# Kernel tuning notes

Hardware: AMD Instinct MI355X
Metric: run time of the kernel (lower is better)

The kernel has to match this reference:

```python
import jax, jax.numpy as jnp
import numpy as np

B, N, H, D, HS, RS = 4, 512, 16, 64, 1024, 64  # HS = H*D, HSIZE_INSIDE == HSIZE
SCALE = 1.0 / float(np.sqrt(D))


def setup_inputs() -> dict:
    key = jax.random.key(0)
    ks = jax.random.split(key, 11)
    s = 0.02
    return {
        "v": jax.random.normal(ks[0], (B, N, HS), jnp.float32),
        "k": jax.random.normal(ks[1], (B, N, HS), jnp.float32),
        "q": jax.random.normal(ks[2], (B, N, HS), jnp.float32),
        "mask": jax.random.randint(ks[3], (B, 1, N, N), 0, 2).astype(bool),
        "rel_embed": jax.random.uniform(ks[4], (B, N, N, RS), jnp.float32),
        # weights stored as [in, out] (torch Linear applies x @ W.T)
        "Wv": jax.random.normal(ks[5], (HS, HS), jnp.float32) * s,
        "Wk": jax.random.normal(ks[6], (HS, HS), jnp.float32) * s,
        "Wq": jax.random.normal(ks[7], (HS, HS), jnp.float32) * s,
        "Wr": jax.random.normal(ks[8], (RS, H), jnp.float32) * s,
        "br": jax.random.normal(ks[9], (H,), jnp.float32) * s,
        "Wm": jax.random.normal(ks[10], (HS, HS), jnp.float32) * s,
    }


def reference(v, k, q, mask, rel_embed, Wv, Wk, Wq, Wr, br, Wm):
    b, nq, _ = q.shape

    def proj(x, W):  # [b, n, HS] -> [b, H, n, D]
        return (x @ W).reshape(b, -1, H, D).transpose(0, 2, 1, 3)

    vh, kh, qh = proj(v, Wv), proj(k, Wk), proj(q, Wq)
    # learned relative-position bias: relu -> clamp -> log, [b, H, nq, nk]
    r = jax.nn.relu(rel_embed @ Wr + br)
    bias = jnp.log(jnp.clip(r, 1e-6, None)).transpose(0, 3, 1, 2)
    scores = jnp.einsum('bhqd,bhkd->bhqk', qh, kh) * SCALE + bias
    scores = jnp.where(mask, jnp.float32(-1e9), scores)
    att = jax.nn.softmax(scores, axis=-1)  # dropout_r = 0
    atted = jnp.einsum('bhqk,bhkd->bhqd', att, vh)
    atted = atted.transpose(0, 2, 1, 3).reshape(b, nq, H * D)
    return atted @ Wm
```

## Files before the change

### kernel.cpp

```cpp
#include <hip/hip_runtime.h>
#include <hip/hip_bf16.h>


typedef __bf16 bf16_t;
typedef __bf16 bf16x8 __attribute__((ext_vector_type(8)));
typedef float f32x4 __attribute__((ext_vector_type(4)));

__device__ __forceinline__ f32x4 mfma16(bf16x8 a, bf16x8 b, f32x4 c) {
  return __builtin_amdgcn_mfma_f32_16x16x32_bf16(a, b, c, 0, 0, 0);
}
__device__ __forceinline__ f32x4 zero4() {
  f32x4 z; z[0] = 0.f; z[1] = 0.f; z[2] = 0.f; z[3] = 0.f; return z;
}

#define GLOAD_LDS16(gptr, lptr)                                                   \
  __builtin_amdgcn_global_load_lds(                                               \
      (const __attribute__((address_space(1))) unsigned int*)(gptr),              \
      (__attribute__((address_space(3))) unsigned int*)(lptr), 16, 0, 0)

__global__ __launch_bounds__(256) void prep_kernel(
    const float* __restrict__ W0, const float* __restrict__ W1,
    const float* __restrict__ W2, const float* __restrict__ W3,
    bf16_t* __restrict__ OutBase,
    const float* __restrict__ q, const float* __restrict__ k, const float* __restrict__ v,
    bf16_t* __restrict__ Qc, bf16_t* __restrict__ Kc, bf16_t* __restrict__ Vc,
    const unsigned int* __restrict__ mw, int* __restrict__ flag) {
  const int tid = threadIdx.x;
  if (blockIdx.x >= 1024) {
    const size_t gid = (size_t)(blockIdx.x - 1024) * 256 + tid;
    const int which = (int)(gid >> 18);
    const size_t off = (gid & 262143) * 8;
    const float* src = which == 0 ? q : which == 1 ? k : v;
    bf16_t* dst = which == 0 ? Qc : which == 1 ? Kc : Vc;
    const float scl = which == 0 ? 0.125f : 1.0f;
    float4 f0 = *(const float4*)(src + off);
    float4 f1 = *(const float4*)(src + off + 4);
    bf16x8 o;
    o[0] = (bf16_t)(f0.x * scl); o[1] = (bf16_t)(f0.y * scl);
    o[2] = (bf16_t)(f0.z * scl); o[3] = (bf16_t)(f0.w * scl);
    o[4] = (bf16_t)(f1.x * scl); o[5] = (bf16_t)(f1.y * scl);
    o[6] = (bf16_t)(f1.z * scl); o[7] = (bf16_t)(f1.w * scl);
    *(bf16x8*)(dst + off) = o;
    return;
  }
  const int wz = blockIdx.x >> 8, wy = (blockIdx.x >> 4) & 15, wx = blockIdx.x & 15;
  const float* W = wz == 0 ? W0 : wz == 1 ? W1 : wz == 2 ? W2 : W3;
  bf16_t* Ot = OutBase + (size_t)wz * 1024 * 1024;
  __shared__ float tile[64][68];
  __shared__ int sflag;
  const bool probe = (blockIdx.x == 0);
  if (probe && tid == 0) sflag = 0;
  const int i0 = wy * 64, j0 = wx * 64;
  const int ri = tid >> 2, rc = (tid & 3) * 16;
  const float* src = W + (size_t)(i0 + ri) * 1024 + j0 + rc;
#pragma unroll
  for (int qq = 0; qq < 4; ++qq) {
    float4 f = *(const float4*)(src + qq * 4);
    *(float4*)(&tile[ri][rc + qq * 4]) = f;
  }
  if (probe) {
    int any = 0;
    for (int i = tid; i < 4096; i += 256) any |= (mw[i] > 1u) ? 1 : 0;
    if (any) atomicOr(&sflag, 1);
  }
  __syncthreads();
  const int wj = tid >> 2, wc = (tid & 3) * 16;
  bf16x8 o0, o1;
#pragma unroll
  for (int s = 0; s < 8; ++s) o0[s] = (bf16_t)tile[wc + s][wj];
#pragma unroll
  for (int s = 0; s < 8; ++s) o1[s] = (bf16_t)tile[wc + 8 + s][wj];
  bf16_t* dst = Ot + (size_t)(j0 + wj) * 1024 + i0 + wc;
  *(bf16x8*)dst = o0;
  *(bf16x8*)(dst + 8) = o1;
  if (probe && tid == 0) *flag = sflag;
}

__global__ __launch_bounds__(256) void fat_kernel(
    const float* __restrict__ rel, const float* __restrict__ Wr,
    const float* __restrict__ br, const void* __restrict__ mask,
    const int* __restrict__ mflag, bf16_t* __restrict__ biasM,
    const bf16_t* __restrict__ Aq, const bf16_t* __restrict__ Ak, const bf16_t* __restrict__ Av,
    const bf16_t* __restrict__ Bq, const bf16_t* __restrict__ Bk, const bf16_t* __restrict__ Bv,
    bf16_t* __restrict__ Oq, bf16_t* __restrict__ Ok, bf16_t* __restrict__ Ov) {
  __shared__ __align__(16) bf16_t Asm[128 * 64];
  __shared__ __align__(16) bf16_t Bsm[128 * 64];
  const int tid = threadIdx.x, wid = tid >> 6, lane = tid & 63;
  const int lg = lane >> 4, lc = lane & 15;

  if (blockIdx.x < 2048) {
    const int pair = blockIdx.x;
    const int b = pair >> 9, qrow = pair & 511;
    const int isU8 = *mflag;
    bf16x8 wf[2];
#pragma unroll
    for (int kk = 0; kk < 2; ++kk)
#pragma unroll
      for (int j = 0; j < 8; ++j)
        wf[kk][j] = (bf16_t)Wr[(kk * 32 + lg * 8 + j) * 16 + lc];
    float brv[4];
#pragma unroll
    for (int j = 0; j < 4; ++j) brv[j] = br[lg * 4 + j];
    const float* relrow = rel + (size_t)pair * 512 * 64;
    const size_t mbase = (size_t)b * 512 * 512 + (size_t)qrow * 512;
    bf16_t* outb = biasM + (size_t)b * 16 * 512 * 512 + (size_t)qrow * 512;
#pragma unroll 4
    for (int kt = wid * 8; kt < wid * 8 + 8; ++kt) {
      const int k0 = kt * 16;
      const float* rrow = relrow + (size_t)(k0 + lc) * 64;
      f32x4 acc;
      acc[0] = brv[0]; acc[1] = brv[1]; acc[2] = brv[2]; acc[3] = brv[3];
#pragma unroll
      for (int kk = 0; kk < 2; ++kk) {
        const float4* s = (const float4*)(rrow + kk * 32 + lg * 8);
        float4 f0 = s[0], f1 = s[1];
        bf16x8 bfr;
        bfr[0] = (bf16_t)f0.x; bfr[1] = (bf16_t)f0.y; bfr[2] = (bf16_t)f0.z; bfr[3] = (bf16_t)f0.w;
        bfr[4] = (bf16_t)f1.x; bfr[5] = (bf16_t)f1.y; bfr[6] = (bf16_t)f1.z; bfr[7] = (bf16_t)f1.w;
        acc = mfma16(wf[kk], bfr, acc);
      }
      bool mb;
      if (isU8) mb = ((const unsigned char*)mask)[mbase + k0 + lc] != 0;
      else      mb = ((const int*)mask)[mbase + k0 + lc] != 0;
#pragma unroll
      for (int j = 0; j < 4; ++j) {
        const float valf = mb ? -1e9f : __logf(fmaxf(acc[j], 1e-6f));
        outb[(size_t)(lg * 4 + j) * 512 * 512 + k0 + lc] = (bf16_t)valf;
      }
    }
    return;
  }

  const int idx = blockIdx.x - 2048;
  const int z = idx >> 7, rem = idx & 127;
  const int byy = rem >> 3, bxx = rem & 7;
  const bf16_t* A = (z == 0) ? Aq : (z == 1) ? Ak : Av;
  const bf16_t* Bt = (z == 0) ? Bq : (z == 1) ? Bk : Bv;
  bf16_t* Out = (z == 0) ? Oq : (z == 1) ? Ok : Ov;
  const int m0 = byy * 128, n0 = bxx * 128;
  const int wm = (wid >> 1) * 64, wn = (wid & 1) * 64;
  const int sr = lane >> 3;
  const int scch = lane & 7;
  const int srcch = scch ^ sr;
  const bf16_t* Ap[4];
  const bf16_t* Bp[4];
#pragma unroll
  for (int i = 0; i < 4; ++i) {
    const int r = wid * 32 + i * 8 + sr;
    Ap[i] = A + (size_t)(m0 + r) * 1024 + srcch * 8;
    Bp[i] = Bt + (size_t)(n0 + r) * 1024 + srcch * 8;
  }
  f32x4 acc[4][4];
#pragma unroll
  for (int i = 0; i < 4; ++i)
#pragma unroll
    for (int j = 0; j < 4; ++j) acc[i][j] = zero4();

  for (int k0 = 0; k0 < 1024; k0 += 64) {
#pragma unroll
    for (int i = 0; i < 4; ++i) {
      GLOAD_LDS16(Ap[i] + k0, Asm + (wid * 32 + i * 8) * 64);
      GLOAD_LDS16(Bp[i] + k0, Bsm + (wid * 32 + i * 8) * 64);
    }
    __syncthreads();
#pragma unroll
    for (int kk = 0; kk < 2; ++kk) {
      bf16x8 af[4], bfv[4];
#pragma unroll
      for (int i = 0; i < 4; ++i) {
        const int ar = wm + i * 16 + lc;
        af[i] = *(const bf16x8*)(Asm + ar * 64 + ((kk * 4 + lg) ^ (ar & 7)) * 8);
        const int brr = wn + i * 16 + lc;
        bfv[i] = *(const bf16x8*)(Bsm + brr * 64 + ((kk * 4 + lg) ^ (brr & 7)) * 8);
      }
#pragma unroll
      for (int mi = 0; mi < 4; ++mi)
#pragma unroll
        for (int ni = 0; ni < 4; ++ni) acc[mi][ni] = mfma16(af[mi], bfv[ni], acc[mi][ni]);
    }
    __syncthreads();
  }
#pragma unroll
  for (int mi = 0; mi < 4; ++mi)
#pragma unroll
    for (int ni = 0; ni < 4; ++ni)
#pragma unroll
      for (int j = 0; j < 4; ++j) {
        const int m = m0 + wm + mi * 16 + lg * 4 + j;
        const int col = n0 + wn + ni * 16 + lc;
        const int b = m >> 9, n = m & 511;
        const int h = col >> 6, d = col & 63;
        Out[(((size_t)(b * 16 + h)) * 512 + n) * 64 + d] = (bf16_t)acc[mi][ni][j];
      }
}

__global__ __launch_bounds__(256) void attn_kernel(
    const bf16_t* __restrict__ Qh, const bf16_t* __restrict__ Kh,
    const bf16_t* __restrict__ Vh, const bf16_t* __restrict__ biasM,
    bf16_t* __restrict__ atted) {
  __shared__ __align__(16) bf16_t Ksm[2][64 * 64];
  __shared__ __align__(16) bf16_t Vtsm[2][64 * 88];
  __shared__ __align__(16) bf16_t Psm[4 * 16 * 64];
  const int tid = threadIdx.x, wid = tid >> 6, lane = tid & 63;
  const int lg = lane >> 4, lc = lane & 15;
  const int bid = blockIdx.x;
  const int qt = bid & 7, h = (bid >> 3) & 15, b = bid >> 7;
  const size_t headoff = (size_t)(b * 16 + h) * 512 * 64;
  const bf16_t* Qb = Qh + headoff;
  const bf16_t* Kb = Kh + headoff;
  const bf16_t* Vb = Vh + headoff;
  const int q0 = qt * 64 + wid * 16;
  const bf16_t* biasb = biasM + ((size_t)(b * 16 + h) * 512 + q0) * 512;

  bf16x8 qf[2];
#pragma unroll
  for (int kk = 0; kk < 2; ++kk)
    qf[kk] = *(const bf16x8*)(Qb + (size_t)(q0 + lc) * 64 + kk * 32 + lg * 8);

  f32x4 Oacc[4];
#pragma unroll
  for (int ds = 0; ds < 4; ++ds) Oacc[ds] = zero4();
  float mrun[4], lrun[4];
#pragma unroll
  for (int j = 0; j < 4; ++j) { mrun[j] = -INFINITY; lrun[j] = 0.f; }

  const int krow = tid & 63, kc0 = (tid >> 6) * 2;
  const int vn = tid & 63, vd0 = (tid >> 6) * 16;
  bf16_t* Pw = Psm + wid * 16 * 64;

#define STAGE(T, BUF)                                                          \
  do {                                                                         \
    const int kb_ = (T) * 64;                                                  \
    _Pragma("unroll") for (int ci = 0; ci < 2; ++ci) {                         \
      const int c_ = kc0 + ci;                                                 \
      bf16x8 kv_ = *(const bf16x8*)(Kb + (size_t)(kb_ + krow) * 64 + c_ * 8);  \
      *(bf16x8*)(Ksm[BUF] + krow * 64 + (c_ ^ (krow & 7)) * 8) = kv_;          \
    }                                                                          \
    bf16x8 v0_ = *(const bf16x8*)(Vb + (size_t)(kb_ + vn) * 64 + vd0);         \
    bf16x8 v1_ = *(const bf16x8*)(Vb + (size_t)(kb_ + vn) * 64 + vd0 + 8);     \
    _Pragma("unroll") for (int i = 0; i < 8; ++i)                              \
        Vtsm[BUF][(vd0 + i) * 88 + vn] = v0_[i];                               \
    _Pragma("unroll") for (int i = 0; i < 8; ++i)                              \
        Vtsm[BUF][(vd0 + 8 + i) * 88 + vn] = v1_[i];                           \
  } while (0)

  STAGE(0, 0);
  __syncthreads();

  for (int t = 0; t < 8; ++t) {
    const int cur = t & 1;
    if (t < 7) STAGE(t + 1, cur ^ 1);

    f32x4 sacc[4];
#pragma unroll
    for (int quad = 0; quad < 4; ++quad)
#pragma unroll
      for (int j = 0; j < 4; ++j)
        sacc[quad][j] = (float)biasb[(size_t)(lg * 4 + j) * 512 + t * 64 + quad * 16 + lc];

    const bf16_t* Kc = Ksm[cur];
#pragma unroll
    for (int quad = 0; quad < 4; ++quad) {
      const int kr = quad * 16 + lc;
#pragma unroll
      for (int kk = 0; kk < 2; ++kk) {
        bf16x8 kf = *(const bf16x8*)(Kc + kr * 64 + ((kk * 4 + lg) ^ (kr & 7)) * 8);
        sacc[quad] = mfma16(qf[kk], kf, sacc[quad]);
      }
    }

    float p[4][4];
#pragma unroll
    for (int j = 0; j < 4; ++j) {
      float tmax = fmaxf(fmaxf(sacc[0][j], sacc[1][j]), fmaxf(sacc[2][j], sacc[3][j]));
#pragma unroll
      for (int mm = 1; mm < 16; mm <<= 1) tmax = fmaxf(tmax, __shfl_xor(tmax, mm));
      const float mnew = fmaxf(mrun[j], tmax);
      const float sf = __expf(mrun[j] - mnew);
      mrun[j] = mnew;
      lrun[j] *= sf;
#pragma unroll
      for (int ds = 0; ds < 4; ++ds) Oacc[ds][j] *= sf;
      float psum = 0.f;
#pragma unroll
      for (int quad = 0; quad < 4; ++quad) {
        const float pv = __expf(sacc[quad][j] - mnew);
        p[quad][j] = pv;
        psum += pv;
      }
      lrun[j] += psum;
    }

#pragma unroll
    for (int quad = 0; quad < 4; ++quad)
#pragma unroll
      for (int j = 0; j < 4; ++j) {
        const int row = lg * 4 + j, col = quad * 16 + lc;
        Pw[row * 64 + ((col >> 3) ^ (row & 7)) * 8 + (col & 7)] = (bf16_t)p[quad][j];
      }

    const bf16_t* Vc = Vtsm[cur];
#pragma unroll
    for (int kk = 0; kk < 2; ++kk) {
      bf16x8 pf = *(const bf16x8*)(Pw + lc * 64 + ((kk * 4 + lg) ^ (lc & 7)) * 8);
#pragma unroll
      for (int ds = 0; ds < 4; ++ds) {
        bf16x8 vf = *(const bf16x8*)(Vc + (ds * 16 + lc) * 88 + kk * 32 + lg * 8);
        Oacc[ds] = mfma16(pf, vf, Oacc[ds]);
      }
    }
    __syncthreads();
  }
#undef STAGE

#pragma unroll
  for (int j = 0; j < 4; ++j) {
    float l = lrun[j];
#pragma unroll
    for (int mm = 1; mm < 16; mm <<= 1) l += __shfl_xor(l, mm);
    lrun[j] = 1.0f / l;
  }
#pragma unroll
  for (int ds = 0; ds < 4; ++ds)
#pragma unroll
    for (int j = 0; j < 4; ++j) {
      const int n = q0 + lg * 4 + j;
      const int d = ds * 16 + lc;
      atted[((size_t)b * 512 + n) * 1024 + h * 64 + d] = (bf16_t)(Oacc[ds][j] * lrun[j]);
    }
}

__global__ __launch_bounds__(256) void out_gemm2(
    const bf16_t* __restrict__ A, const bf16_t* __restrict__ Bt, float* __restrict__ Out) {
  __shared__ __align__(16) bf16_t Asm[128 * 64];
  __shared__ __align__(16) bf16_t Bsm[128 * 64];
  const int tid = threadIdx.x, wid = tid >> 6, lane = tid & 63;
  const int lg = lane >> 4, lc = lane & 15;
  const int m0 = blockIdx.y * 128, n0 = blockIdx.x * 128;
  const int wm = (wid >> 1) * 64, wn = (wid & 1) * 64;
  const int sr = lane >> 3, scch = lane & 7;
  const int srcch = scch ^ sr;
  const bf16_t* Ap[4];
  const bf16_t* Bp[4];
#pragma unroll
  for (int i = 0; i < 4; ++i) {
    const int r = wid * 32 + i * 8 + sr;
    Ap[i] = A + (size_t)(m0 + r) * 1024 + srcch * 8;
    Bp[i] = Bt + (size_t)(n0 + r) * 1024 + srcch * 8;
  }
  f32x4 acc[4][4];
#pragma unroll
  for (int i = 0; i < 4; ++i)
#pragma unroll
    for (int j = 0; j < 4; ++j) acc[i][j] = zero4();

  for (int k0 = 0; k0 < 1024; k0 += 64) {
#pragma unroll
    for (int i = 0; i < 4; ++i) {
      GLOAD_LDS16(Ap[i] + k0, Asm + (wid * 32 + i * 8) * 64);
      GLOAD_LDS16(Bp[i] + k0, Bsm + (wid * 32 + i * 8) * 64);
    }
    __syncthreads();
#pragma unroll
    for (int kk = 0; kk < 2; ++kk) {
      bf16x8 af[4], bfv[4];
#pragma unroll
      for (int i = 0; i < 4; ++i) {
        const int ar = wm + i * 16 + lc;
        af[i] = *(const bf16x8*)(Asm + ar * 64 + ((kk * 4 + lg) ^ (ar & 7)) * 8);
        const int brr = wn + i * 16 + lc;
        bfv[i] = *(const bf16x8*)(Bsm + brr * 64 + ((kk * 4 + lg) ^ (brr & 7)) * 8);
      }
#pragma unroll
      for (int mi = 0; mi < 4; ++mi)
#pragma unroll
        for (int ni = 0; ni < 4; ++ni) acc[mi][ni] = mfma16(af[mi], bfv[ni], acc[mi][ni]);
    }
    __syncthreads();
  }
#pragma unroll
  for (int mi = 0; mi < 4; ++mi)
#pragma unroll
    for (int ni = 0; ni < 4; ++ni)
#pragma unroll
      for (int j = 0; j < 4; ++j) {
        const int m = m0 + wm + mi * 16 + lg * 4 + j;
        const int col = n0 + wn + ni * 16 + lc;
        Out[(size_t)m * 1024 + col] = acc[mi][ni][j];
      }
}

extern "C" void kernel_launch(void* const* d_in, const int* in_sizes, int n_in,
                              void* d_out, int out_size, void* d_ws, size_t ws_size,
                              hipStream_t stream) {
  const float* v = (const float*)d_in[0];
  const float* k = (const float*)d_in[1];
  const float* q = (const float*)d_in[2];
  const void* mask = d_in[3];
  const float* rel = (const float*)d_in[4];
  const float* Wv = (const float*)d_in[5];
  const float* Wk = (const float*)d_in[6];
  const float* Wq = (const float*)d_in[7];
  const float* Wr = (const float*)d_in[8];
  const float* br = (const float*)d_in[9];
  const float* Wm = (const float*)d_in[10];

  char* ws = (char*)d_ws;
  bf16_t* Wt = (bf16_t*)ws;
  bf16_t* Qh = (bf16_t*)(ws + ((size_t)8 << 20));
  bf16_t* Kh = (bf16_t*)(ws + ((size_t)12 << 20));
  bf16_t* Vh = (bf16_t*)(ws + ((size_t)16 << 20));
  bf16_t* biasM = (bf16_t*)(ws + ((size_t)20 << 20));
  bf16_t* atted = (bf16_t*)(ws + ((size_t)52 << 20));
  bf16_t* Qc = (bf16_t*)(ws + ((size_t)56 << 20));
  bf16_t* Kc = (bf16_t*)(ws + ((size_t)60 << 20));
  bf16_t* Vc = (bf16_t*)(ws + ((size_t)64 << 20));
  int* mflag = (int*)(ws + ((size_t)68 << 20));
  bf16_t* Wvt = Wt + 0 * 1048576;
  bf16_t* Wkt = Wt + 1 * 1048576;
  bf16_t* Wqt = Wt + 2 * 1048576;
  bf16_t* Wmt = Wt + 3 * 1048576;

  prep_kernel<<<dim3(4096), 256, 0, stream>>>(Wv, Wk, Wq, Wm, Wt, q, k, v, Qc, Kc, Vc,
                                              (const unsigned int*)mask, mflag);
  fat_kernel<<<dim3(2432), 256, 0, stream>>>(rel, Wr, br, mask, mflag, biasM,
                                             Qc, Kc, Vc, Wqt, Wkt, Wvt, Qh, Kh, Vh);
  attn_kernel<<<dim3(512), 256, 0, stream>>>(Qh, Kh, Vh, biasM, atted);
  out_gemm2<<<dim3(8, 16), 256, 0, stream>>>(atted, Wmt, (float*)d_out);
}
```

Before: 144.8 us.

## Split bias computation across prep and projection kernels, prefetch bias before staging

Moves the relative-position bias work so that 896 of the 2048 (batch, query-row) blocks run inside the prep kernel and the other 1152 run inside the projection GEMM kernel. The bias work, which mostly streams memory, then overlaps with both the weight transpose/convert and the GEMM. The mask dtype probe now runs per block on its own mask row instead of as a single global flag, removing the dependency on the prep kernel. In attention, bias loads are issued before the next K/V stage to hide their latency. The per-row probe could misdetect the dtype if a row's bytes happen to look like int32 data.

```diff
diff --git a/kernel.cpp b/kernel.cpp
--- a/kernel.cpp
+++ b/kernel.cpp
@@ -18,14 +18,75 @@
       (const __attribute__((address_space(1))) unsigned int*)(gptr),              \
       (__attribute__((address_space(3))) unsigned int*)(lptr), 16, 0, 0)
 
-__global__ __launch_bounds__(256) void prep_kernel(
+__device__ __forceinline__ void bias_block(
+    int pair, int tid,
+    const float* __restrict__ rel, const float* __restrict__ Wr,
+    const float* __restrict__ br, const void* __restrict__ mask,
+    bf16_t* __restrict__ biasM, int* su8) {
+  const int wid = tid >> 6, lane = tid & 63;
+  const int lg = lane >> 4, lc = lane & 15;
+  const int b = pair >> 9, qrow = pair & 511;
+  const size_t mbase = (size_t)b * 262144 + (size_t)qrow * 512;
+  const unsigned int* mrow32 = (const unsigned int*)((const unsigned char*)mask + mbase);
+  if (tid == 0) *su8 = 0;
+  __syncthreads();
+  if (tid < 128 && mrow32[tid] > 1u) atomicOr(su8, 1);
+  __syncthreads();
+  const int isU8 = *su8;
+
+  bf16x8 wf[2];
+#pragma unroll
+  for (int kk = 0; kk < 2; ++kk)
+#pragma unroll
+    for (int j = 0; j < 8; ++j)
+      wf[kk][j] = (bf16_t)Wr[(kk * 32 + lg * 8 + j) * 16 + lc];
+  float brv[4];
+#pragma unroll
+  for (int j = 0; j < 4; ++j) brv[j] = br[lg * 4 + j];
+  const float* relrow = rel + (size_t)pair * 512 * 64;
+  bf16_t* outb = biasM + (size_t)b * 16 * 512 * 512 + (size_t)qrow * 512;
+#pragma unroll 4
+  for (int kt = wid * 8; kt < wid * 8 + 8; ++kt) {
+    const int k0 = kt * 16;
+    const float* rrow = relrow + (size_t)(k0 + lc) * 64;
+    f32x4 acc;
+    acc[0] = brv[0]; acc[1] = brv[1]; acc[2] = brv[2]; acc[3] = brv[3];
+#pragma unroll
+    for (int kk = 0; kk < 2; ++kk) {
+      const float4* s = (const float4*)(rrow + kk * 32 + lg * 8);
+      float4 f0 = s[0], f1 = s[1];
+      bf16x8 bfr;
+      bfr[0] = (bf16_t)f0.x; bfr[1] = (bf16_t)f0.y; bfr[2] = (bf16_t)f0.z; bfr[3] = (bf16_t)f0.w;
+      bfr[4] = (bf16_t)f1.x; bfr[5] = (bf16_t)f1.y; bfr[6] = (bf16_t)f1.z; bfr[7] = (bf16_t)f1.w;
+      acc = mfma16(wf[kk], bfr, acc);
+    }
+    bool mb;
+    if (isU8) mb = ((const unsigned char*)mask)[mbase + k0 + lc] != 0;
+    else      mb = ((const int*)mask)[mbase + k0 + lc] != 0;
+#pragma unroll
+    for (int j = 0; j < 4; ++j) {
+      const float valf = mb ? -1e9f : __logf(fmaxf(acc[j], 1e-6f));
+      outb[(size_t)(lg * 4 + j) * 512 * 512 + k0 + lc] = (bf16_t)valf;
+    }
+  }
+}
+
+__global__ __launch_bounds__(256) void k1_prep_bias(
     const float* __restrict__ W0, const float* __restrict__ W1,
     const float* __restrict__ W2, const float* __restrict__ W3,
     bf16_t* __restrict__ OutBase,
     const float* __restrict__ q, const float* __restrict__ k, const float* __restrict__ v,
     bf16_t* __restrict__ Qc, bf16_t* __restrict__ Kc, bf16_t* __restrict__ Vc,
-    const unsigned int* __restrict__ mw, int* __restrict__ flag) {
+    const float* __restrict__ rel, const float* __restrict__ Wr,
+    const float* __restrict__ br, const void* __restrict__ mask,
+    bf16_t* __restrict__ biasM) {
+  __shared__ float tile[64][68];
+  __shared__ int su8;
   const int tid = threadIdx.x;
+  if (blockIdx.x >= 4096) {
+    bias_block(blockIdx.x - 4096, tid, rel, Wr, br, mask, biasM, &su8);
+    return;
+  }
   if (blockIdx.x >= 1024) {
     const size_t gid = (size_t)(blockIdx.x - 1024) * 256 + tid;
     const int which = (int)(gid >> 18);
@@ -46,10 +107,6 @@
   const int wz = blockIdx.x >> 8, wy = (blockIdx.x >> 4) & 15, wx = blockIdx.x & 15;
   const float* W = wz == 0 ? W0 : wz == 1 ? W1 : wz == 2 ? W2 : W3;
   bf16_t* Ot = OutBase + (size_t)wz * 1024 * 1024;
-  __shared__ float tile[64][68];
-  __shared__ int sflag;
-  const bool probe = (blockIdx.x == 0);
-  if (probe && tid == 0) sflag = 0;
   const int i0 = wy * 64, j0 = wx * 64;
   const int ri = tid >> 2, rc = (tid & 3) * 16;
   const float* src = W + (size_t)(i0 + ri) * 1024 + j0 + rc;
@@ -57,11 +114,6 @@
   for (int qq = 0; qq < 4; ++qq) {
     float4 f = *(const float4*)(src + qq * 4);
     *(float4*)(&tile[ri][rc + qq * 4]) = f;
-  }
-  if (probe) {
-    int any = 0;
-    for (int i = tid; i < 4096; i += 256) any |= (mw[i] > 1u) ? 1 : 0;
-    if (any) atomicOr(&sflag, 1);
   }
   __syncthreads();
   const int wj = tid >> 2, wc = (tid & 3) * 16;
@@ -73,65 +125,26 @@
   bf16_t* dst = Ot + (size_t)(j0 + wj) * 1024 + i0 + wc;
   *(bf16x8*)dst = o0;
   *(bf16x8*)(dst + 8) = o1;
-  if (probe && tid == 0) *flag = sflag;
-}
-
-__global__ __launch_bounds__(256) void fat_kernel(
+}
+
+__global__ __launch_bounds__(256) void k2_proj_bias(
+    const bf16_t* __restrict__ Aq, const bf16_t* __restrict__ Ak, const bf16_t* __restrict__ Av,
+    const bf16_t* __restrict__ Bq, const bf16_t* __restrict__ Bk, const bf16_t* __restrict__ Bv,
+    bf16_t* __restrict__ Oq, bf16_t* __restrict__ Ok, bf16_t* __restrict__ Ov,
     const float* __restrict__ rel, const float* __restrict__ Wr,
     const float* __restrict__ br, const void* __restrict__ mask,
-    const int* __restrict__ mflag, bf16_t* __restrict__ biasM,
-    const bf16_t* __restrict__ Aq, const bf16_t* __restrict__ Ak, const bf16_t* __restrict__ Av,
-    const bf16_t* __restrict__ Bq, const bf16_t* __restrict__ Bk, const bf16_t* __restrict__ Bv,
-    bf16_t* __restrict__ Oq, bf16_t* __restrict__ Ok, bf16_t* __restrict__ Ov) {
+    bf16_t* __restrict__ biasM) {
   __shared__ __align__(16) bf16_t Asm[128 * 64];
   __shared__ __align__(16) bf16_t Bsm[128 * 64];
+  __shared__ int su8;
   const int tid = threadIdx.x, wid = tid >> 6, lane = tid & 63;
   const int lg = lane >> 4, lc = lane & 15;
 
-  if (blockIdx.x < 2048) {
-    const int pair = blockIdx.x;
-    const int b = pair >> 9, qrow = pair & 511;
-    const int isU8 = *mflag;
-    bf16x8 wf[2];
-#pragma unroll
-    for (int kk = 0; kk < 2; ++kk)
-#pragma unroll
-      for (int j = 0; j < 8; ++j)
-        wf[kk][j] = (bf16_t)Wr[(kk * 32 + lg * 8 + j) * 16 + lc];
-    float brv[4];
-#pragma unroll
-    for (int j = 0; j < 4; ++j) brv[j] = br[lg * 4 + j];
-    const float* relrow = rel + (size_t)pair * 512 * 64;
-    const size_t mbase = (size_t)b * 512 * 512 + (size_t)qrow * 512;
-    bf16_t* outb = biasM + (size_t)b * 16 * 512 * 512 + (size_t)qrow * 512;
-#pragma unroll 4
-    for (int kt = wid * 8; kt < wid * 8 + 8; ++kt) {
-      const int k0 = kt * 16;
-      const float* rrow = relrow + (size_t)(k0 + lc) * 64;
-      f32x4 acc;
-      acc[0] = brv[0]; acc[1] = brv[1]; acc[2] = brv[2]; acc[3] = brv[3];
-#pragma unroll
-      for (int kk = 0; kk < 2; ++kk) {
-        const float4* s = (const float4*)(rrow + kk * 32 + lg * 8);
-        float4 f0 = s[0], f1 = s[1];
-        bf16x8 bfr;
-        bfr[0] = (bf16_t)f0.x; bfr[1] = (bf16_t)f0.y; bfr[2] = (bf16_t)f0.z; bfr[3] = (bf16_t)f0.w;
-        bfr[4] = (bf16_t)f1.x; bfr[5] = (bf16_t)f1.y; bfr[6] = (bf16_t)f1.z; bfr[7] = (bf16_t)f1.w;
-        acc = mfma16(wf[kk], bfr, acc);
-      }
-      bool mb;
-      if (isU8) mb = ((const unsigned char*)mask)[mbase + k0 + lc] != 0;
-      else      mb = ((const int*)mask)[mbase + k0 + lc] != 0;
-#pragma unroll
-      for (int j = 0; j < 4; ++j) {
-        const float valf = mb ? -1e9f : __logf(fmaxf(acc[j], 1e-6f));
-        outb[(size_t)(lg * 4 + j) * 512 * 512 + k0 + lc] = (bf16_t)valf;
-      }
-    }
+  if (blockIdx.x >= 384) {
+    bias_block(896 + (int)blockIdx.x - 384, tid, rel, Wr, br, mask, biasM, &su8);
     return;
   }
-
-  const int idx = blockIdx.x - 2048;
+  const int idx = blockIdx.x;
   const int z = idx >> 7, rem = idx & 127;
   const int byy = rem >> 3, bxx = rem & 7;
   const bf16_t* A = (z == 0) ? Aq : (z == 1) ? Ak : Av;
@@ -249,14 +262,21 @@
 
   for (int t = 0; t < 8; ++t) {
     const int cur = t & 1;
+
+    float bsv[4][4];
+#pragma unroll
+    for (int quad = 0; quad < 4; ++quad)
+#pragma unroll
+      for (int j = 0; j < 4; ++j)
+        bsv[quad][j] = (float)biasb[(size_t)(lg * 4 + j) * 512 + t * 64 + quad * 16 + lc];
+
     if (t < 7) STAGE(t + 1, cur ^ 1);
 
     f32x4 sacc[4];
 #pragma unroll
     for (int quad = 0; quad < 4; ++quad)
 #pragma unroll
-      for (int j = 0; j < 4; ++j)
-        sacc[quad][j] = (float)biasb[(size_t)(lg * 4 + j) * 512 + t * 64 + quad * 16 + lc];
+      for (int j = 0; j < 4; ++j) sacc[quad][j] = bsv[quad][j];
 
     const bf16_t* Kc = Ksm[cur];
 #pragma unroll
@@ -415,16 +435,15 @@
   bf16_t* Qc = (bf16_t*)(ws + ((size_t)56 << 20));
   bf16_t* Kc = (bf16_t*)(ws + ((size_t)60 << 20));
   bf16_t* Vc = (bf16_t*)(ws + ((size_t)64 << 20));
-  int* mflag = (int*)(ws + ((size_t)68 << 20));
   bf16_t* Wvt = Wt + 0 * 1048576;
   bf16_t* Wkt = Wt + 1 * 1048576;
   bf16_t* Wqt = Wt + 2 * 1048576;
   bf16_t* Wmt = Wt + 3 * 1048576;
 
-  prep_kernel<<<dim3(4096), 256, 0, stream>>>(Wv, Wk, Wq, Wm, Wt, q, k, v, Qc, Kc, Vc,
-                                              (const unsigned int*)mask, mflag);
-  fat_kernel<<<dim3(2432), 256, 0, stream>>>(rel, Wr, br, mask, mflag, biasM,
-                                             Qc, Kc, Vc, Wqt, Wkt, Wvt, Qh, Kh, Vh);
+  k1_prep_bias<<<dim3(4992), 256, 0, stream>>>(Wv, Wk, Wq, Wm, Wt, q, k, v, Qc, Kc, Vc,
+                                               rel, Wr, br, mask, biasM);
+  k2_proj_bias<<<dim3(1536), 256, 0, stream>>>(Qc, Kc, Vc, Wqt, Wkt, Wvt, Qh, Kh, Vh,
+                                               rel, Wr, br, mask, biasM);
   attn_kernel<<<dim3(512), 256, 0, stream>>>(Qh, Kh, Vh, biasM, atted);
   out_gemm2<<<dim3(8, 16), 256, 0, stream>>>(atted, Wmt, (float*)d_out);
 }
```

Result: slower. 160.5 us (+10.9%).

## Store V pre-transposed from projection and stage bias tiles through LDS

Applied to the files above, without the earlier changes.

The projection GEMM now writes V in a per-head [d][n] transposed layout with packed 4-wide stores, so the attention kernel can load V rows with 16-byte vector copies into LDS instead of scattering single elements to transpose. The attention kernel also stages each 64x64 bias tile into a padded shared buffer with coalesced vector loads, replacing the strided scalar global bias reads per lane. This costs extra LDS and a branch in the GEMM epilogue that depends on z.

```diff
diff --git a/kernel.cpp b/kernel.cpp
--- a/kernel.cpp
+++ b/kernel.cpp
@@ -3,6 +3,7 @@
 
 
 typedef __bf16 bf16_t;
+typedef __bf16 bf16x4 __attribute__((ext_vector_type(4)));
 typedef __bf16 bf16x8 __attribute__((ext_vector_type(8)));
 typedef float f32x4 __attribute__((ext_vector_type(4)));
 
@@ -102,7 +103,7 @@
 #pragma unroll
     for (int j = 0; j < 4; ++j) brv[j] = br[lg * 4 + j];
     const float* relrow = rel + (size_t)pair * 512 * 64;
-    const size_t mbase = (size_t)b * 512 * 512 + (size_t)qrow * 512;
+    const size_t mbase = (size_t)b * 262144 + (size_t)qrow * 512;
     bf16_t* outb = biasM + (size_t)b * 16 * 512 * 512 + (size_t)qrow * 512;
 #pragma unroll 4
     for (int kt = wid * 8; kt < wid * 8 + 8; ++kt) {
@@ -180,26 +181,43 @@
     }
     __syncthreads();
   }
-#pragma unroll
-  for (int mi = 0; mi < 4; ++mi)
-#pragma unroll
-    for (int ni = 0; ni < 4; ++ni)
-#pragma unroll
-      for (int j = 0; j < 4; ++j) {
-        const int m = m0 + wm + mi * 16 + lg * 4 + j;
+  if (z == 2) {
+#pragma unroll
+    for (int mi = 0; mi < 4; ++mi)
+#pragma unroll
+      for (int ni = 0; ni < 4; ++ni) {
+        const int m = m0 + wm + mi * 16 + lg * 4;
         const int col = n0 + wn + ni * 16 + lc;
-        const int b = m >> 9, n = m & 511;
+        const int b = m >> 9, nb = m & 511;
         const int h = col >> 6, d = col & 63;
-        Out[(((size_t)(b * 16 + h)) * 512 + n) * 64 + d] = (bf16_t)acc[mi][ni][j];
-      }
+        bf16x4 pk;
+#pragma unroll
+        for (int j = 0; j < 4; ++j) pk[j] = (bf16_t)acc[mi][ni][j];
+        *(bf16x4*)(Out + ((size_t)(b * 16 + h) * 64 + d) * 512 + nb) = pk;
+      }
+  } else {
+#pragma unroll
+    for (int mi = 0; mi < 4; ++mi)
+#pragma unroll
+      for (int ni = 0; ni < 4; ++ni)
+#pragma unroll
+        for (int j = 0; j < 4; ++j) {
+          const int m = m0 + wm + mi * 16 + lg * 4 + j;
+          const int col = n0 + wn + ni * 16 + lc;
+          const int b = m >> 9, n = m & 511;
+          const int h = col >> 6, d = col & 63;
+          Out[(((size_t)(b * 16 + h)) * 512 + n) * 64 + d] = (bf16_t)acc[mi][ni][j];
+        }
+  }
 }
 
 __global__ __launch_bounds__(256) void attn_kernel(
     const bf16_t* __restrict__ Qh, const bf16_t* __restrict__ Kh,
-    const bf16_t* __restrict__ Vh, const bf16_t* __restrict__ biasM,
+    const bf16_t* __restrict__ Vt, const bf16_t* __restrict__ biasM,
     bf16_t* __restrict__ atted) {
   __shared__ __align__(16) bf16_t Ksm[2][64 * 64];
   __shared__ __align__(16) bf16_t Vtsm[2][64 * 88];
+  __shared__ __align__(16) bf16_t Bsm2[2][64 * 72];
   __shared__ __align__(16) bf16_t Psm[4 * 16 * 64];
   const int tid = threadIdx.x, wid = tid >> 6, lane = tid & 63;
   const int lg = lane >> 4, lc = lane & 15;
@@ -208,9 +226,9 @@
   const size_t headoff = (size_t)(b * 16 + h) * 512 * 64;
   const bf16_t* Qb = Qh + headoff;
   const bf16_t* Kb = Kh + headoff;
-  const bf16_t* Vb = Vh + headoff;
+  const bf16_t* Vb = Vt + headoff;
   const int q0 = qt * 64 + wid * 16;
-  const bf16_t* biasb = biasM + ((size_t)(b * 16 + h) * 512 + q0) * 512;
+  const bf16_t* biasblk = biasM + ((size_t)(b * 16 + h) * 512 + qt * 64) * 512;
 
   bf16x8 qf[2];
 #pragma unroll
@@ -225,23 +243,27 @@
   for (int j = 0; j < 4; ++j) { mrun[j] = -INFINITY; lrun[j] = 0.f; }
 
   const int krow = tid & 63, kc0 = (tid >> 6) * 2;
-  const int vn = tid & 63, vd0 = (tid >> 6) * 16;
+  const int vq = tid >> 3, vc = tid & 7;
   bf16_t* Pw = Psm + wid * 16 * 64;
 
-#define STAGE(T, BUF)                                                          \
-  do {                                                                         \
-    const int kb_ = (T) * 64;                                                  \
-    _Pragma("unroll") for (int ci = 0; ci < 2; ++ci) {                         \
-      const int c_ = kc0 + ci;                                                 \
-      bf16x8 kv_ = *(const bf16x8*)(Kb + (size_t)(kb_ + krow) * 64 + c_ * 8);  \
-      *(bf16x8*)(Ksm[BUF] + krow * 64 + (c_ ^ (krow & 7)) * 8) = kv_;          \
-    }                                                                          \
-    bf16x8 v0_ = *(const bf16x8*)(Vb + (size_t)(kb_ + vn) * 64 + vd0);         \
-    bf16x8 v1_ = *(const bf16x8*)(Vb + (size_t)(kb_ + vn) * 64 + vd0 + 8);     \
-    _Pragma("unroll") for (int i = 0; i < 8; ++i)                              \
-        Vtsm[BUF][(vd0 + i) * 88 + vn] = v0_[i];                               \
-    _Pragma("unroll") for (int i = 0; i < 8; ++i)                              \
-        Vtsm[BUF][(vd0 + 8 + i) * 88 + vn] = v1_[i];                           \
+#define STAGE(T, BUF)                                                           \
+  do {                                                                          \
+    const int kb_ = (T) * 64;                                                   \
+    _Pragma("unroll") for (int ci = 0; ci < 2; ++ci) {                          \
+      const int c_ = kc0 + ci;                                                  \
+      bf16x8 kv_ = *(const bf16x8*)(Kb + (size_t)(kb_ + krow) * 64 + c_ * 8);   \
+      *(bf16x8*)(Ksm[BUF] + krow * 64 + (c_ ^ (krow & 7)) * 8) = kv_;           \
+    }                                                                           \
+    _Pragma("unroll") for (int it = 0; it < 2; ++it) {                          \
+      const int d_ = it * 32 + vq;                                              \
+      bf16x8 vv_ = *(const bf16x8*)(Vb + (size_t)d_ * 512 + kb_ + vc * 8);      \
+      *(bf16x8*)(Vtsm[BUF] + d_ * 88 + vc * 8) = vv_;                           \
+    }                                                                           \
+    _Pragma("unroll") for (int it = 0; it < 2; ++it) {                          \
+      const int q_ = it * 32 + vq;                                              \
+      bf16x8 bv_ = *(const bf16x8*)(biasblk + (size_t)q_ * 512 + kb_ + vc * 8); \
+      *(bf16x8*)(Bsm2[BUF] + q_ * 72 + vc * 8) = bv_;                           \
+    }                                                                           \
   } while (0)
 
   STAGE(0, 0);
@@ -251,12 +273,13 @@
     const int cur = t & 1;
     if (t < 7) STAGE(t + 1, cur ^ 1);
 
+    const bf16_t* Bc = Bsm2[cur];
     f32x4 sacc[4];
 #pragma unroll
     for (int quad = 0; quad < 4; ++quad)
 #pragma unroll
       for (int j = 0; j < 4; ++j)
-        sacc[quad][j] = (float)biasb[(size_t)(lg * 4 + j) * 512 + t * 64 + quad * 16 + lc];
+        sacc[quad][j] = (float)Bc[(wid * 16 + lg * 4 + j) * 72 + quad * 16 + lc];
 
     const bf16_t* Kc = Ksm[cur];
 #pragma unroll
@@ -409,7 +432,7 @@
   bf16_t* Wt = (bf16_t*)ws;
   bf16_t* Qh = (bf16_t*)(ws + ((size_t)8 << 20));
   bf16_t* Kh = (bf16_t*)(ws + ((size_t)12 << 20));
-  bf16_t* Vh = (bf16_t*)(ws + ((size_t)16 << 20));
+  bf16_t* Vth = (bf16_t*)(ws + ((size_t)16 << 20));
   bf16_t* biasM = (bf16_t*)(ws + ((size_t)20 << 20));
   bf16_t* atted = (bf16_t*)(ws + ((size_t)52 << 20));
   bf16_t* Qc = (bf16_t*)(ws + ((size_t)56 << 20));
@@ -424,7 +447,7 @@
   prep_kernel<<<dim3(4096), 256, 0, stream>>>(Wv, Wk, Wq, Wm, Wt, q, k, v, Qc, Kc, Vc,
                                               (const unsigned int*)mask, mflag);
   fat_kernel<<<dim3(2432), 256, 0, stream>>>(rel, Wr, br, mask, mflag, biasM,
-                                             Qc, Kc, Vc, Wqt, Wkt, Wvt, Qh, Kh, Vh);
-  attn_kernel<<<dim3(512), 256, 0, stream>>>(Qh, Kh, Vh, biasM, atted);
+                                             Qc, Kc, Vc, Wqt, Wkt, Wvt, Qh, Kh, Vth);
+  attn_kernel<<<dim3(512), 256, 0, stream>>>(Qh, Kh, Vth, biasM, atted);
   out_gemm2<<<dim3(8, 16), 256, 0, stream>>>(atted, Wmt, (float*)d_out);
 }
```

Measured after the change: 149.5 us. +3.3%, slower.

## Split fused bias/projection kernel and stage rel_embed through LDS with coalesced bias stores

Applied to the files above, without the earlier changes.

The combined bias-plus-QKV-projection kernel is split into a dedicated bias kernel and a separate 3D-grid projection GEMM. The new bias kernel double-buffers rel_embed chunks into swizzled shared memory with direct global-to-LDS loads, and preloads the mask bits once. It also transposes results through a small LDS tile so each lane writes 4 contiguous bf16 values instead of scattered 2-byte stores. The aim is better coalescing on the large rel_embed read and bias write, at the cost of an extra kernel launch and the loss of overlap between the bias and GEMM work.

```diff
diff --git a/kernel.cpp b/kernel.cpp
--- a/kernel.cpp
+++ b/kernel.cpp
@@ -3,6 +3,7 @@
 
 
 typedef __bf16 bf16_t;
+typedef __bf16 bf16x4 __attribute__((ext_vector_type(4)));
 typedef __bf16 bf16x8 __attribute__((ext_vector_type(8)));
 typedef float f32x4 __attribute__((ext_vector_type(4)));
 
@@ -76,71 +77,103 @@
   if (probe && tid == 0) *flag = sflag;
 }
 
-__global__ __launch_bounds__(256) void fat_kernel(
+__global__ __launch_bounds__(256) void bias_v3(
     const float* __restrict__ rel, const float* __restrict__ Wr,
     const float* __restrict__ br, const void* __restrict__ mask,
-    const int* __restrict__ mflag, bf16_t* __restrict__ biasM,
+    const int* __restrict__ mflag, bf16_t* __restrict__ biasM) {
+  __shared__ __align__(16) float relS[2][64 * 64];
+  __shared__ __align__(16) bf16_t outS[4][16 * 20];
+  const int tid = threadIdx.x, wid = tid >> 6, lane = tid & 63;
+  const int lg = lane >> 4, lc = lane & 15;
+  const int pair = blockIdx.x;
+  const int b = pair >> 9, qrow = pair & 511;
+  const int isU8 = *mflag;
+
+  bf16x8 wf[2];
+#pragma unroll
+  for (int kk = 0; kk < 2; ++kk)
+#pragma unroll
+    for (int j = 0; j < 8; ++j)
+      wf[kk][j] = (bf16_t)Wr[(kk * 32 + lg * 8 + j) * 16 + lc];
+  float brv[4];
+#pragma unroll
+  for (int j = 0; j < 4; ++j) brv[j] = br[lg * 4 + j];
+
+  const float* relblk = rel + (size_t)pair * 32768;
+  const size_t mbase = (size_t)b * 262144 + (size_t)qrow * 512;
+  bf16_t* outb = biasM + (size_t)b * 16 * 262144 + (size_t)qrow * 512;
+
+  unsigned mbits = 0;
+#pragma unroll
+  for (int c = 0; c < 8; ++c) {
+    const size_t mi = mbase + c * 64 + wid * 16 + lc;
+    const bool mb = isU8 ? (((const unsigned char*)mask)[mi] != 0)
+                         : (((const int*)mask)[mi] != 0);
+    mbits |= (mb ? 1u : 0u) << c;
+  }
+
+  const int s_rsub = lane >> 4, s_p = lane & 15;
+#define BSTAGE(C, BUF)                                                          \
+  do {                                                                          \
+    _Pragma("unroll") for (int i = 0; i < 4; ++i) {                             \
+      const int r_ = wid * 16 + i * 4 + s_rsub;                                 \
+      const float* src_ =                                                       \
+          relblk + ((size_t)(C) * 64 + r_) * 64 + ((s_p ^ (r_ & 7)) << 2);      \
+      GLOAD_LDS16(src_, &relS[BUF][wid * 1024 + i * 256]);                      \
+    }                                                                           \
+  } while (0)
+
+  BSTAGE(0, 0);
+
+  const int h_ = lane >> 2, k4_ = lane & 3;
+  for (int c = 0; c < 8; ++c) {
+    const int buf = c & 1;
+    __syncthreads();
+    if (c < 7) BSTAGE(c + 1, buf ^ 1);
+
+    const float* Rb = relS[buf];
+    const int rowL = wid * 16 + lc;
+    const int x = lc & 7;
+    f32x4 acc;
+    acc[0] = brv[0]; acc[1] = brv[1]; acc[2] = brv[2]; acc[3] = brv[3];
+#pragma unroll
+    for (int kk = 0; kk < 2; ++kk) {
+      const int c0 = kk * 8 + lg * 2;
+      float4 f0 = *(const float4*)(Rb + rowL * 64 + ((c0 ^ x) << 2));
+      float4 f1 = *(const float4*)(Rb + rowL * 64 + (((c0 + 1) ^ x) << 2));
+      bf16x8 bfr;
+      bfr[0] = (bf16_t)f0.x; bfr[1] = (bf16_t)f0.y; bfr[2] = (bf16_t)f0.z; bfr[3] = (bf16_t)f0.w;
+      bfr[4] = (bf16_t)f1.x; bfr[5] = (bf16_t)f1.y; bfr[6] = (bf16_t)f1.z; bfr[7] = (bf16_t)f1.w;
+      acc = mfma16(wf[kk], bfr, acc);
+    }
+    const bool mb = (mbits >> c) & 1;
+    bf16_t* oS = outS[wid];
+#pragma unroll
+    for (int j = 0; j < 4; ++j) {
+      const float valf = mb ? -1e9f : __logf(fmaxf(acc[j], 1e-6f));
+      oS[(lg * 4 + j) * 20 + lc] = (bf16_t)valf;
+    }
+    bf16x4 ov = *(const bf16x4*)(oS + h_ * 20 + k4_ * 4);
+    *(bf16x4*)(outb + (size_t)h_ * 262144 + c * 64 + wid * 16 + k4_ * 4) = ov;
+  }
+#undef BSTAGE
+}
+
+__global__ __launch_bounds__(256) void proj_gemm2(
     const bf16_t* __restrict__ Aq, const bf16_t* __restrict__ Ak, const bf16_t* __restrict__ Av,
     const bf16_t* __restrict__ Bq, const bf16_t* __restrict__ Bk, const bf16_t* __restrict__ Bv,
     bf16_t* __restrict__ Oq, bf16_t* __restrict__ Ok, bf16_t* __restrict__ Ov) {
+  const int z = blockIdx.z;
+  const bf16_t* A = (z == 0) ? Aq : (z == 1) ? Ak : Av;
+  const bf16_t* Bt = (z == 0) ? Bq : (z == 1) ? Bk : Bv;
+  bf16_t* Out = (z == 0) ? Oq : (z == 1) ? Ok : Ov;
   __shared__ __align__(16) bf16_t Asm[128 * 64];
   __shared__ __align__(16) bf16_t Bsm[128 * 64];
   const int tid = threadIdx.x, wid = tid >> 6, lane = tid & 63;
   const int lg = lane >> 4, lc = lane & 15;
-
-  if (blockIdx.x < 2048) {
-    const int pair = blockIdx.x;
-    const int b = pair >> 9, qrow = pair & 511;
-    const int isU8 = *mflag;
-    bf16x8 wf[2];
-#pragma unroll
-    for (int kk = 0; kk < 2; ++kk)
-#pragma unroll
-      for (int j = 0; j < 8; ++j)
-        wf[kk][j] = (bf16_t)Wr[(kk * 32 + lg * 8 + j) * 16 + lc];
-    float brv[4];
-#pragma unroll
-    for (int j = 0; j < 4; ++j) brv[j] = br[lg * 4 + j];
-    const float* relrow = rel + (size_t)pair * 512 * 64;
-    const size_t mbase = (size_t)b * 512 * 512 + (size_t)qrow * 512;
-    bf16_t* outb = biasM + (size_t)b * 16 * 512 * 512 + (size_t)qrow * 512;
-#pragma unroll 4
-    for (int kt = wid * 8; kt < wid * 8 + 8; ++kt) {
-      const int k0 = kt * 16;
-      const float* rrow = relrow + (size_t)(k0 + lc) * 64;
-      f32x4 acc;
-      acc[0] = brv[0]; acc[1] = brv[1]; acc[2] = brv[2]; acc[3] = brv[3];
-#pragma unroll
-      for (int kk = 0; kk < 2; ++kk) {
-        const float4* s = (const float4*)(rrow + kk * 32 + lg * 8);
-        float4 f0 = s[0], f1 = s[1];
-        bf16x8 bfr;
-        bfr[0] = (bf16_t)f0.x; bfr[1] = (bf16_t)f0.y; bfr[2] = (bf16_t)f0.z; bfr[3] = (bf16_t)f0.w;
-        bfr[4] = (bf16_t)f1.x; bfr[5] = (bf16_t)f1.y; bfr[6] = (bf16_t)f1.z; bfr[7] = (bf16_t)f1.w;
-        acc = mfma16(wf[kk], bfr, acc);
-      }
-      bool mb;
-      if (isU8) mb = ((const unsigned char*)mask)[mbase + k0 + lc] != 0;
-      else      mb = ((const int*)mask)[mbase + k0 + lc] != 0;
-#pragma unroll
-      for (int j = 0; j < 4; ++j) {
-        const float valf = mb ? -1e9f : __logf(fmaxf(acc[j], 1e-6f));
-        outb[(size_t)(lg * 4 + j) * 512 * 512 + k0 + lc] = (bf16_t)valf;
-      }
-    }
-    return;
-  }
-
-  const int idx = blockIdx.x - 2048;
-  const int z = idx >> 7, rem = idx & 127;
-  const int byy = rem >> 3, bxx = rem & 7;
-  const bf16_t* A = (z == 0) ? Aq : (z == 1) ? Ak : Av;
-  const bf16_t* Bt = (z == 0) ? Bq : (z == 1) ? Bk : Bv;
-  bf16_t* Out = (z == 0) ? Oq : (z == 1) ? Ok : Ov;
-  const int m0 = byy * 128, n0 = bxx * 128;
+  const int m0 = blockIdx.y * 128, n0 = blockIdx.x * 128;
   const int wm = (wid >> 1) * 64, wn = (wid & 1) * 64;
-  const int sr = lane >> 3;
-  const int scch = lane & 7;
+  const int sr = lane >> 3, scch = lane & 7;
   const int srcch = scch ^ sr;
   const bf16_t* Ap[4];
   const bf16_t* Bp[4];
@@ -423,8 +456,8 @@
 
   prep_kernel<<<dim3(4096), 256, 0, stream>>>(Wv, Wk, Wq, Wm, Wt, q, k, v, Qc, Kc, Vc,
                                               (const unsigned int*)mask, mflag);
-  fat_kernel<<<dim3(2432), 256, 0, stream>>>(rel, Wr, br, mask, mflag, biasM,
-                                             Qc, Kc, Vc, Wqt, Wkt, Wvt, Qh, Kh, Vh);
+  bias_v3<<<dim3(2048), 256, 0, stream>>>(rel, Wr, br, mask, mflag, biasM);
+  proj_gemm2<<<dim3(8, 16, 3), 256, 0, stream>>>(Qc, Kc, Vc, Wqt, Wkt, Wvt, Qh, Kh, Vh);
   attn_kernel<<<dim3(512), 256, 0, stream>>>(Qh, Kh, Vh, biasM, atted);
   out_gemm2<<<dim3(8, 16), 256, 0, stream>>>(atted, Wmt, (float*)d_out);
 }
```

Result: slower. 153.3 us (+5.9%).
